# Kernel optimization log

Measured on AMD Instinct MI355X. Metric: run time of the kernel, lower is better.

## Reference

```python
import jax, jax.numpy as jnp
import numpy as np

NUM_HEADS = 16
DIM_IN = 1024
DIM_HIDDEN = 1024
DIM_OUT = 1024
DIM_HEAD = DIM_HIDDEN // NUM_HEADS


def setup_inputs() -> dict:
    key = jax.random.key(0)
    kx, kw1, kw2 = jax.random.split(key, 3)
    B, L = 4, 2048
    x = jax.random.normal(kx, (B, L, DIM_IN), dtype=jnp.float32)
    # xavier_uniform for qkv weight: shape (3*dim_hidden, dim_in) in torch; keep torch layout
    limit_qkv = float(np.sqrt(6.0 / (DIM_IN + 3 * DIM_HIDDEN)))
    W_qkv = jax.random.uniform(kw1, (3 * DIM_HIDDEN, DIM_IN), dtype=jnp.float32,
                               minval=-limit_qkv, maxval=limit_qkv)
    b_qkv = jnp.zeros((3 * DIM_HIDDEN,), dtype=jnp.float32)
    limit_out = float(np.sqrt(6.0 / (DIM_HIDDEN + DIM_OUT)))
    W_out = jax.random.uniform(kw2, (DIM_OUT, DIM_HIDDEN), dtype=jnp.float32,
                               minval=-limit_out, maxval=limit_out)
    b_out = jnp.zeros((DIM_OUT,), dtype=jnp.float32)
    return {"x": x, "W_qkv": W_qkv, "b_qkv": b_qkv, "W_out": W_out, "b_out": b_out}


def reference(x, W_qkv, b_qkv, W_out, b_out):
    B, L, _ = x.shape
    # fused qkv projection: (B, L, 3*dim_hidden)
    qkv = jnp.einsum('bld,ed->ble', x, W_qkv) + b_qkv
    # faithful reshape: (B, L, H, 3*dim_head) then permute to (B, H, L, 3*dim_head)
    qkv = qkv.reshape(B, L, NUM_HEADS, 3 * DIM_HEAD).transpose(0, 2, 1, 3)
    q, k, v = jnp.split(qkv, 3, axis=-1)  # each (B, H, L, dim_head)
    scores = jnp.einsum('bhqd,bhkd->bhqk', q, k) / jnp.sqrt(jnp.float32(DIM_HEAD))
    attn = jax.nn.softmax(scores, axis=-1)
    logits = jnp.einsum('bhqk,bhkd->bhqd', attn, v)
    logits = logits.transpose(0, 2, 1, 3).reshape(B, L, DIM_HIDDEN)
    out = jnp.einsum('blh,oh->blo', logits, W_out) + b_out
    return out
```

## Files before the change

### kernel.cpp

```cpp
#include <hip/hip_runtime.h>
#include <hip/hip_bf16.h>


typedef __attribute__((ext_vector_type(8))) short short8;
typedef __attribute__((ext_vector_type(4))) float f32x4;
typedef __attribute__((ext_vector_type(4))) unsigned int uint32x4;

#define DEV static __device__ __forceinline__

DEV unsigned short f2bf(float f) {
  __hip_bfloat16 h = __float2bfloat16(f);
  return __builtin_bit_cast(unsigned short, h);
}

DEV unsigned int cvt_pk_bf16(float lo, float hi) {
  unsigned int r;
  asm("v_cvt_pk_bf16_f32 %0, %1, %2" : "=v"(r) : "v"(lo), "v"(hi));
  return r;
}

#define PLS32(a, b) asm("v_permlane32_swap_b32 %0, %1" : "+v"(a), "+v"(b))
#define PLS16(a, b) asm("v_permlane16_swap_b32 %0, %1" : "+v"(a), "+v"(b))

DEV void gld_lds16(void* lds, const void* g) {
  __builtin_amdgcn_global_load_lds(
      (const __attribute__((address_space(1))) unsigned int*)g,
      (__attribute__((address_space(3))) unsigned int*)lds, 16, 0, 0);
}

DEV f32x4 mfma16(short8 a, short8 b, f32x4 c) {
  return __builtin_amdgcn_mfma_f32_16x16x32_bf16(a, b, c, 0, 0, 0);
}

__global__ __launch_bounds__(256) void k_cvt3(const float* __restrict__ x,
                                              const float* __restrict__ wq,
                                              const float* __restrict__ wo,
                                              unsigned short* __restrict__ dx,
                                              unsigned short* __restrict__ dwq,
                                              unsigned short* __restrict__ dwo) {
  int i = blockIdx.x * 256 + threadIdx.x;
  const float* s;
  unsigned short* d;
  if (i < 2097152) {
    s = x; d = dx;
  } else if (i < 2883584) {
    i -= 2097152; s = wq; d = dwq;
  } else {
    i -= 2883584; s = wo; d = dwo;
  }
  float4 v = ((const float4*)s)[i];
  ushort4 o;
  o.x = f2bf(v.x); o.y = f2bf(v.y); o.z = f2bf(v.z); o.w = f2bf(v.w);
  ((ushort4*)d)[i] = o;
}

__global__ __launch_bounds__(256) void k_gemm_qkv(
    const unsigned short* __restrict__ A, const unsigned short* __restrict__ Bw,
    const float* __restrict__ bias,
    unsigned short* __restrict__ Qg, unsigned short* __restrict__ Kg,
    unsigned short* __restrict__ Vg) {
  __shared__ unsigned short As[128 * 64];
  __shared__ unsigned short Bs[128 * 64];
  const int tid = threadIdx.x, lane = tid & 63, w = tid >> 6;
  const int m0 = blockIdx.y * 128, n0 = blockIdx.x * 128;
  const int wr = w >> 1, wc = w & 1;
  const int col = lane & 15, kg = lane >> 4;
  f32x4 acc[4][4] = {};
  const int K = 1024;
  const int st_row = lane >> 3;
  const int st_cb = (lane & 7) * 16;
  const int xr = (col & 7) << 4;
  const int x0 = (kg * 16) ^ xr;
  const int x1 = (64 + kg * 16) ^ xr;
  for (int k0 = 0; k0 < K; k0 += 64) {
#pragma unroll
    for (int j = 0; j < 4; ++j) {
      const int rr = (j * 4 + w) * 8;
      const int row = rr + st_row;
      const int sc = st_cb ^ ((row & 7) << 4);
      gld_lds16((char*)As + rr * 128, (const char*)(A + (size_t)(m0 + row) * K + k0) + sc);
      gld_lds16((char*)Bs + rr * 128, (const char*)(Bw + (size_t)(n0 + row) * K + k0) + sc);
    }
    __syncthreads();
    short8 bfr[4][2];
#pragma unroll
    for (int ni = 0; ni < 4; ni++) {
      const char* bb = (const char*)Bs + (wc * 64 + ni * 16 + col) * 128;
      bfr[ni][0] = *(const short8*)(bb + x0);
      bfr[ni][1] = *(const short8*)(bb + x1);
    }
#pragma unroll
    for (int mi = 0; mi < 4; mi++) {
      const char* ab = (const char*)As + (wr * 64 + mi * 16 + col) * 128;
      const short8 af0 = *(const short8*)(ab + x0);
      const short8 af1 = *(const short8*)(ab + x1);
#pragma unroll
      for (int ni = 0; ni < 4; ni++) {
        acc[mi][ni] = mfma16(af0, bfr[ni][0], acc[mi][ni]);
        acc[mi][ni] = mfma16(af1, bfr[ni][1], acc[mi][ni]);
      }
    }
    __syncthreads();
  }
  const float QSCALE = 0.1803368801111204f;
#pragma unroll
  for (int mi = 0; mi < 4; mi++) {
#pragma unroll
    for (int ni = 0; ni < 4; ni++) {
#pragma unroll
      for (int r = 0; r < 4; r++) {
        const int grow = m0 + wr * 64 + mi * 16 + kg * 4 + r;
        const int gcol = n0 + wc * 64 + ni * 16 + col;
        float v = acc[mi][ni][r] + bias[gcol];
        const int h = gcol / 192, c = gcol % 192;
        const int bh = (grow >> 11) * 16 + h;
        const size_t base = ((size_t)bh * 2048 + (grow & 2047)) * 64;
        if (c < 64) Qg[base + c] = f2bf(v * QSCALE);
        else if (c < 128) Kg[base + (c - 64)] = f2bf(v);
        else Vg[base + (c - 128)] = f2bf(v);
      }
    }
  }
}

__global__ __launch_bounds__(256) void k_transpose(const unsigned short* __restrict__ V,
                                                   unsigned short* __restrict__ Vt) {
  __shared__ unsigned short t[64][72];
  const int tid = threadIdx.x;
  const int bh = blockIdx.y, l0 = blockIdx.x * 64;
#pragma unroll
  for (int i = 0; i < 2; i++) {
    const int slot = i * 256 + tid;
    const int r = slot >> 3, c0 = (slot & 7) * 8;
    short8 v = *(const short8*)(V + ((size_t)bh * 2048 + l0 + r) * 64 + c0);
#pragma unroll
    for (int j = 0; j < 8; j++) t[c0 + j][r] = (unsigned short)v[j];
  }
  __syncthreads();
#pragma unroll
  for (int i = 0; i < 2; i++) {
    const int slot = i * 256 + tid;
    const int d = slot >> 3, x0 = (slot & 7) * 8;
    short8 o;
#pragma unroll
    for (int j = 0; j < 8; j++) o[j] = (short)t[d][x0 + j];
    *(short8*)(Vt + ((size_t)bh * 64 + d) * 2048 + l0 + x0) = o;
  }
}

__global__ __launch_bounds__(256, 3) void k_attn(const unsigned short* __restrict__ Qg,
                                                 const unsigned short* __restrict__ Kg,
                                                 const unsigned short* __restrict__ Vtg,
                                                 unsigned short* __restrict__ Lg) {
  __shared__ unsigned short Ks[2][64 * 64];
  __shared__ unsigned short Vs[2][64 * 64];
  const int tid = threadIdx.x, lane = tid & 63, w = tid >> 6;

  const int id = blockIdx.x + (blockIdx.y << 4);
  const int xcd = id & 7, slot = id >> 3;
  const int bh = ((slot >> 4) << 3) + xcd;
  const int q0 = (slot & 15) * 128 + w * 32;
  const int col = lane & 15, kg = lane >> 4;

  short8 qa[2][2];
#pragma unroll
  for (int sub = 0; sub < 2; sub++) {
    const unsigned short* qbase = Qg + ((size_t)bh * 2048 + q0 + sub * 16 + col) * 64 + kg * 8;
    qa[sub][0] = *(const short8*)(qbase);
    qa[sub][1] = *(const short8*)(qbase + 32);
  }

  f32x4 accO[2][4] = {};
  f32x4 accSum[2] = {};
  const short8 ones = {(short)0x3F80, (short)0x3F80, (short)0x3F80, (short)0x3F80,
                       (short)0x3F80, (short)0x3F80, (short)0x3F80, (short)0x3F80};

  const int st_row8 = lane >> 3;
  const int st_cb = (lane & 7) * 16;

  auto STAGE = [&](int buf, int kt) {
#pragma unroll
    for (int j = 0; j < 2; ++j) {
      const int rr = (j * 4 + w) * 8;
      const int row = rr + st_row8;
      const int sc = st_cb ^ ((row & 7) << 4);
      gld_lds16((char*)&Ks[buf][0] + rr * 128,
                (const char*)(Kg + ((size_t)bh * 2048 + kt * 64 + row) * 64) + sc);
      gld_lds16((char*)&Vs[buf][0] + rr * 128,
                (const char*)(Vtg + ((size_t)bh * 64 + row) * 2048 + (size_t)kt * 64) + sc);
    }
  };

  STAGE(0, 0);

  const int xr = (col & 7) << 4;
  const int x0 = (kg * 16) ^ xr;
  const int x1 = (64 + kg * 16) ^ xr;

  for (int kt = 0; kt < 32; ++kt) {
    const int cur = kt & 1;
    __syncthreads();
    if (kt < 31) STAGE(cur ^ 1, kt + 1);

    const char* KsB = (const char*)&Ks[cur][0];
    const char* VsB = (const char*)&Vs[cur][0];

    short8 kf[4][2];
#pragma unroll
    for (int n = 0; n < 4; n++) {
      const char* kb = KsB + (n * 16 + col) * 128;
      kf[n][0] = *(const short8*)(kb + x0);
      kf[n][1] = *(const short8*)(kb + x1);
    }

    short8 pa[2][2];
#pragma unroll
    for (int sub = 0; sub < 2; sub++) {
      f32x4 s[4];
      __builtin_amdgcn_s_setprio(1);
#pragma unroll
      for (int n = 0; n < 4; n++) {
        s[n] = f32x4{0.f, 0.f, 0.f, 0.f};
        s[n] = mfma16(kf[n][0], qa[sub][0], s[n]);
        s[n] = mfma16(kf[n][1], qa[sub][1], s[n]);
      }
      __builtin_amdgcn_s_setprio(0);
      unsigned int wv[4][2];
#pragma unroll
      for (int n = 0; n < 4; n++) {
        const float p0 = __builtin_amdgcn_exp2f(s[n][0]);
        const float p1 = __builtin_amdgcn_exp2f(s[n][1]);
        const float p2 = __builtin_amdgcn_exp2f(s[n][2]);
        const float p3 = __builtin_amdgcn_exp2f(s[n][3]);
        wv[n][0] = cvt_pk_bf16(p0, p1);
        wv[n][1] = cvt_pk_bf16(p2, p3);
      }
      PLS32(wv[0][0], wv[1][0]);
      PLS32(wv[0][1], wv[1][1]);
      PLS16(wv[0][0], wv[1][0]);
      PLS16(wv[0][1], wv[1][1]);
      PLS32(wv[2][0], wv[3][0]);
      PLS32(wv[2][1], wv[3][1]);
      PLS16(wv[2][0], wv[3][0]);
      PLS16(wv[2][1], wv[3][1]);
      uint32x4 u0 = {wv[0][0], wv[0][1], wv[1][0], wv[1][1]};
      uint32x4 u1 = {wv[2][0], wv[2][1], wv[3][0], wv[3][1]};
      pa[sub][0] = __builtin_bit_cast(short8, u0);
      pa[sub][1] = __builtin_bit_cast(short8, u1);
    }

    __builtin_amdgcn_s_setprio(1);
#pragma unroll
    for (int df = 0; df < 4; df++) {
      const char* vb = VsB + (df * 16 + col) * 128;
      const short8 vf0 = *(const short8*)(vb + x0);
      const short8 vf1 = *(const short8*)(vb + x1);
      accO[0][df] = mfma16(pa[0][0], vf0, accO[0][df]);
      accO[0][df] = mfma16(pa[0][1], vf1, accO[0][df]);
      accO[1][df] = mfma16(pa[1][0], vf0, accO[1][df]);
      accO[1][df] = mfma16(pa[1][1], vf1, accO[1][df]);
    }
#pragma unroll
    for (int sub = 0; sub < 2; sub++) {
      accSum[sub] = mfma16(pa[sub][0], ones, accSum[sub]);
      accSum[sub] = mfma16(pa[sub][1], ones, accSum[sub]);
    }
    __builtin_amdgcn_s_setprio(0);
  }

  const int b = bh >> 4, h = bh & 15;
#pragma unroll
  for (int sub = 0; sub < 2; sub++) {
#pragma unroll
    for (int r = 0; r < 4; r++) {
      const float inv = 1.0f / accSum[sub][r];
      const int grow = q0 + sub * 16 + kg * 4 + r;
      unsigned short* orow = Lg + ((size_t)b * 2048 + grow) * 1024 + h * 64;
#pragma unroll
      for (int df = 0; df < 4; df++) orow[df * 16 + col] = f2bf(accO[sub][df][r] * inv);
    }
  }
}

__global__ __launch_bounds__(256) void k_gemm_out(
    const unsigned short* __restrict__ A, const unsigned short* __restrict__ Bw,
    const float* __restrict__ bias, float* __restrict__ C) {
  __shared__ unsigned short As[128 * 64];
  __shared__ unsigned short Bs[128 * 64];
  const int tid = threadIdx.x, lane = tid & 63, w = tid >> 6;
  const int m0 = blockIdx.y * 128, n0 = blockIdx.x * 128;
  const int wr = w >> 1, wc = w & 1;
  const int col = lane & 15, kg = lane >> 4;
  f32x4 acc[4][4] = {};
  const int K = 1024;
  const int st_row = lane >> 3;
  const int st_cb = (lane & 7) * 16;
  const int xr = (col & 7) << 4;
  const int x0 = (kg * 16) ^ xr;
  const int x1 = (64 + kg * 16) ^ xr;
  for (int k0 = 0; k0 < K; k0 += 64) {
#pragma unroll
    for (int j = 0; j < 4; ++j) {
      const int rr = (j * 4 + w) * 8;
      const int row = rr + st_row;
      const int sc = st_cb ^ ((row & 7) << 4);
      gld_lds16((char*)As + rr * 128, (const char*)(A + (size_t)(m0 + row) * K + k0) + sc);
      gld_lds16((char*)Bs + rr * 128, (const char*)(Bw + (size_t)(n0 + row) * K + k0) + sc);
    }
    __syncthreads();
    short8 bfr[4][2];
#pragma unroll
    for (int ni = 0; ni < 4; ni++) {
      const char* bb = (const char*)Bs + (wc * 64 + ni * 16 + col) * 128;
      bfr[ni][0] = *(const short8*)(bb + x0);
      bfr[ni][1] = *(const short8*)(bb + x1);
    }
#pragma unroll
    for (int mi = 0; mi < 4; mi++) {
      const char* ab = (const char*)As + (wr * 64 + mi * 16 + col) * 128;
      const short8 af0 = *(const short8*)(ab + x0);
      const short8 af1 = *(const short8*)(ab + x1);
#pragma unroll
      for (int ni = 0; ni < 4; ni++) {
        acc[mi][ni] = mfma16(af0, bfr[ni][0], acc[mi][ni]);
        acc[mi][ni] = mfma16(af1, bfr[ni][1], acc[mi][ni]);
      }
    }
    __syncthreads();
  }
#pragma unroll
  for (int mi = 0; mi < 4; mi++) {
#pragma unroll
    for (int ni = 0; ni < 4; ni++) {
#pragma unroll
      for (int r = 0; r < 4; r++) {
        const int grow = m0 + wr * 64 + mi * 16 + kg * 4 + r;
        const int gcol = n0 + wc * 64 + ni * 16 + col;
        C[(size_t)grow * 1024 + gcol] = acc[mi][ni][r] + bias[gcol];
      }
    }
  }
}

extern "C" void kernel_launch(void* const* d_in, const int* in_sizes, int n_in,
                              void* d_out, int out_size, void* d_ws, size_t ws_size,
                              hipStream_t stream) {
  (void)in_sizes; (void)n_in; (void)out_size; (void)ws_size;
  const float* x    = (const float*)d_in[0];
  const float* Wqkv = (const float*)d_in[1];
  const float* bqkv = (const float*)d_in[2];
  const float* Wout = (const float*)d_in[3];
  const float* bout = (const float*)d_in[4];
  float* out = (float*)d_out;

  char* ws = (char*)d_ws;
  unsigned short* Xb  = (unsigned short*)(ws);
  unsigned short* Wqb = (unsigned short*)(ws + 16777216);
  unsigned short* Wob = (unsigned short*)(ws + 23068672);
  unsigned short* Qg  = (unsigned short*)(ws + 25165824);
  unsigned short* Kg  = (unsigned short*)(ws + 41943040);
  unsigned short* Vg  = (unsigned short*)(ws + 58720256);
  unsigned short* Vt  = (unsigned short*)(ws + 75497472);
  unsigned short* Lg  = Xb;

  k_cvt3<<<12288, 256, 0, stream>>>(x, Wqkv, Wout, Xb, Wqb, Wob);
  k_gemm_qkv<<<dim3(24, 64), 256, 0, stream>>>(Xb, Wqb, bqkv, Qg, Kg, Vg);
  k_transpose<<<dim3(32, 64), 256, 0, stream>>>(Vg, Vt);
  k_attn<<<dim3(16, 64), 256, 0, stream>>>(Qg, Kg, Vt, Lg);
  k_gemm_out<<<dim3(8, 64), 256, 0, stream>>>(Lg, Wob, bout, out);
}
```

Before: 195.1 us.

## Double-buffer LDS tiles in both GEMMs and streamline QKV epilogue

Both the QKV and output-projection GEMMs now hold two LDS buffers, and the next k-tile is issued as an async global-to-LDS load while the current tile feeds the MFMAs. This removes one barrier per iteration and overlaps load latency with compute. The QKV epilogue also hoists the head/section decode, bias and scale out of the per-row loop. In exchange LDS per block doubles to 64KB, which may reduce occupancy. Correctness relies on the single barrier per iteration ordering the async loads against reuse of the alternate buffer.

Result: faster. 187.0 us (-4.2%).

```diff
diff --git a/kernel.cpp b/kernel.cpp
--- a/kernel.cpp
+++ b/kernel.cpp
@@ -59,8 +59,8 @@
     const float* __restrict__ bias,
     unsigned short* __restrict__ Qg, unsigned short* __restrict__ Kg,
     unsigned short* __restrict__ Vg) {
-  __shared__ unsigned short As[128 * 64];
-  __shared__ unsigned short Bs[128 * 64];
+  __shared__ unsigned short As[2][128 * 64];
+  __shared__ unsigned short Bs[2][128 * 64];
   const int tid = threadIdx.x, lane = tid & 63, w = tid >> 6;
   const int m0 = blockIdx.y * 128, n0 = blockIdx.x * 128;
   const int wr = w >> 1, wc = w & 1;
@@ -72,26 +72,39 @@
   const int xr = (col & 7) << 4;
   const int x0 = (kg * 16) ^ xr;
   const int x1 = (64 + kg * 16) ^ xr;
-  for (int k0 = 0; k0 < K; k0 += 64) {
+
+  auto STAGE = [&](int buf, int k0) {
 #pragma unroll
     for (int j = 0; j < 4; ++j) {
       const int rr = (j * 4 + w) * 8;
       const int row = rr + st_row;
       const int sc = st_cb ^ ((row & 7) << 4);
-      gld_lds16((char*)As + rr * 128, (const char*)(A + (size_t)(m0 + row) * K + k0) + sc);
-      gld_lds16((char*)Bs + rr * 128, (const char*)(Bw + (size_t)(n0 + row) * K + k0) + sc);
-    }
+      gld_lds16((char*)&As[buf][0] + rr * 128,
+                (const char*)(A + (size_t)(m0 + row) * K + k0) + sc);
+      gld_lds16((char*)&Bs[buf][0] + rr * 128,
+                (const char*)(Bw + (size_t)(n0 + row) * K + k0) + sc);
+    }
+  };
+
+  STAGE(0, 0);
+
+  for (int kk = 0; kk < 16; ++kk) {
+    const int cur = kk & 1;
     __syncthreads();
+    if (kk < 15) STAGE(cur ^ 1, (kk + 1) * 64);
+
+    const char* AsB = (const char*)&As[cur][0];
+    const char* BsB = (const char*)&Bs[cur][0];
     short8 bfr[4][2];
 #pragma unroll
     for (int ni = 0; ni < 4; ni++) {
-      const char* bb = (const char*)Bs + (wc * 64 + ni * 16 + col) * 128;
+      const char* bb = BsB + (wc * 64 + ni * 16 + col) * 128;
       bfr[ni][0] = *(const short8*)(bb + x0);
       bfr[ni][1] = *(const short8*)(bb + x1);
     }
 #pragma unroll
     for (int mi = 0; mi < 4; mi++) {
-      const char* ab = (const char*)As + (wr * 64 + mi * 16 + col) * 128;
+      const char* ab = AsB + (wr * 64 + mi * 16 + col) * 128;
       const short8 af0 = *(const short8*)(ab + x0);
       const short8 af1 = *(const short8*)(ab + x1);
 #pragma unroll
@@ -100,24 +113,29 @@
         acc[mi][ni] = mfma16(af1, bfr[ni][1], acc[mi][ni]);
       }
     }
-    __syncthreads();
-  }
+  }
+
   const float QSCALE = 0.1803368801111204f;
-#pragma unroll
-  for (int mi = 0; mi < 4; mi++) {
-#pragma unroll
-    for (int ni = 0; ni < 4; ni++) {
+  const int b = m0 >> 11;
+  const int l0 = (m0 & 2047) + wr * 64;
+#pragma unroll
+  for (int ni = 0; ni < 4; ni++) {
+    const int gcol = n0 + wc * 64 + ni * 16 + col;
+    const int h = gcol / 192, c = gcol % 192;
+    const float bv = bias[gcol];
+    unsigned short* __restrict__ dst;
+    int off;
+    float scl;
+    if (c < 64) { dst = Qg; off = c; scl = QSCALE; }
+    else if (c < 128) { dst = Kg; off = c - 64; scl = 1.0f; }
+    else { dst = Vg; off = c - 128; scl = 1.0f; }
+    unsigned short* __restrict__ hp = dst + ((size_t)(b * 16 + h) * 2048) * 64 + off;
+#pragma unroll
+    for (int mi = 0; mi < 4; mi++) {
 #pragma unroll
       for (int r = 0; r < 4; r++) {
-        const int grow = m0 + wr * 64 + mi * 16 + kg * 4 + r;
-        const int gcol = n0 + wc * 64 + ni * 16 + col;
-        float v = acc[mi][ni][r] + bias[gcol];
-        const int h = gcol / 192, c = gcol % 192;
-        const int bh = (grow >> 11) * 16 + h;
-        const size_t base = ((size_t)bh * 2048 + (grow & 2047)) * 64;
-        if (c < 64) Qg[base + c] = f2bf(v * QSCALE);
-        else if (c < 128) Kg[base + (c - 64)] = f2bf(v);
-        else Vg[base + (c - 128)] = f2bf(v);
+        const int l = l0 + mi * 16 + kg * 4 + r;
+        hp[(size_t)l * 64] = f2bf((acc[mi][ni][r] + bv) * scl);
       }
     }
   }
@@ -285,8 +303,8 @@
 __global__ __launch_bounds__(256) void k_gemm_out(
     const unsigned short* __restrict__ A, const unsigned short* __restrict__ Bw,
     const float* __restrict__ bias, float* __restrict__ C) {
-  __shared__ unsigned short As[128 * 64];
-  __shared__ unsigned short Bs[128 * 64];
+  __shared__ unsigned short As[2][128 * 64];
+  __shared__ unsigned short Bs[2][128 * 64];
   const int tid = threadIdx.x, lane = tid & 63, w = tid >> 6;
   const int m0 = blockIdx.y * 128, n0 = blockIdx.x * 128;
   const int wr = w >> 1, wc = w & 1;
@@ -298,26 +316,39 @@
   const int xr = (col & 7) << 4;
   const int x0 = (kg * 16) ^ xr;
   const int x1 = (64 + kg * 16) ^ xr;
-  for (int k0 = 0; k0 < K; k0 += 64) {
+
+  auto STAGE = [&](int buf, int k0) {
 #pragma unroll
     for (int j = 0; j < 4; ++j) {
       const int rr = (j * 4 + w) * 8;
       const int row = rr + st_row;
       const int sc = st_cb ^ ((row & 7) << 4);
-      gld_lds16((char*)As + rr * 128, (const char*)(A + (size_t)(m0 + row) * K + k0) + sc);
-      gld_lds16((char*)Bs + rr * 128, (const char*)(Bw + (size_t)(n0 + row) * K + k0) + sc);
-    }
+      gld_lds16((char*)&As[buf][0] + rr * 128,
+                (const char*)(A + (size_t)(m0 + row) * K + k0) + sc);
+      gld_lds16((char*)&Bs[buf][0] + rr * 128,
+                (const char*)(Bw + (size_t)(n0 + row) * K + k0) + sc);
+    }
+  };
+
+  STAGE(0, 0);
+
+  for (int kk = 0; kk < 16; ++kk) {
+    const int cur = kk & 1;
     __syncthreads();
+    if (kk < 15) STAGE(cur ^ 1, (kk + 1) * 64);
+
+    const char* AsB = (const char*)&As[cur][0];
+    const char* BsB = (const char*)&Bs[cur][0];
     short8 bfr[4][2];
 #pragma unroll
     for (int ni = 0; ni < 4; ni++) {
-      const char* bb = (const char*)Bs + (wc * 64 + ni * 16 + col) * 128;
+      const char* bb = BsB + (wc * 64 + ni * 16 + col) * 128;
       bfr[ni][0] = *(const short8*)(bb + x0);
       bfr[ni][1] = *(const short8*)(bb + x1);
     }
 #pragma unroll
     for (int mi = 0; mi < 4; mi++) {
-      const char* ab = (const char*)As + (wr * 64 + mi * 16 + col) * 128;
+      const char* ab = AsB + (wr * 64 + mi * 16 + col) * 128;
       const short8 af0 = *(const short8*)(ab + x0);
       const short8 af1 = *(const short8*)(ab + x1);
 #pragma unroll
@@ -326,8 +357,8 @@
         acc[mi][ni] = mfma16(af1, bfr[ni][1], acc[mi][ni]);
       }
     }
-    __syncthreads();
-  }
+  }
+
 #pragma unroll
   for (int mi = 0; mi < 4; mi++) {
 #pragma unroll
```
